# Kernel optimization log

Hardware: AMD Instinct MI355X
Metric: run time of the kernel (lower is better)

## Reference

```python
import jax, jax.numpy as jnp
import numpy as np

N_NODES = 10000
N_EDGES = 640000
IN_DIM, HID_DIM, OUT_DIM = 128, 512, 512


def setup_inputs() -> dict:
    key = jax.random.key(0)
    k1, k2, k3, k4, k5, k6 = jax.random.split(key, 6)
    feat = jax.random.normal(k1, (N_NODES, IN_DIM), dtype=jnp.float32)
    edge_index = jax.random.randint(k2, (2, N_EDGES), 0, N_NODES, dtype=jnp.int64)
    s1 = 1.0 / np.sqrt(IN_DIM)
    s2 = 1.0 / np.sqrt(HID_DIM)
    W1 = jax.random.uniform(k3, (IN_DIM, HID_DIM), jnp.float32, -s1, s1)
    b1 = jnp.zeros((HID_DIM,), jnp.float32)
    W2 = jax.random.uniform(k4, (HID_DIM, OUT_DIM), jnp.float32, -s2, s2)
    b2 = jnp.zeros((OUT_DIM,), jnp.float32)
    return {"feat": feat, "edge_index": edge_index, "W1": W1, "b1": b1, "W2": W2, "b2": b2}


def _degree_norms(edge_index, n_nodes):
    src, dst = edge_index[0], edge_index[1]
    ones = jnp.ones((edge_index.shape[1],), jnp.float32)
    out_deg = jax.ops.segment_sum(ones, src, num_segments=n_nodes)
    in_deg = jax.ops.segment_sum(ones, dst, num_segments=n_nodes)
    # DGL clamps degree to >= 1 to avoid division by zero
    norm_src = jax.lax.rsqrt(jnp.maximum(out_deg, 1.0))  # [N]
    norm_dst = jax.lax.rsqrt(jnp.maximum(in_deg, 1.0))   # [N]
    return norm_src, norm_dst


def _graph_conv(x, src, dst, norm_src, norm_dst, W, b, n_nodes):
    # norm='both': D_in^{-1/2} A D_out^{-1/2} X W + b
    x = x * norm_src[:, None]
    agg = jax.ops.segment_sum(x[src], dst, num_segments=n_nodes)  # [N, d]
    agg = agg * norm_dst[:, None]
    return agg @ W + b


def reference(feat, edge_index, W1, b1, W2, b2):
    n = feat.shape[0]
    src, dst = edge_index[0], edge_index[1]
    norm_src, norm_dst = _degree_norms(edge_index, n)
    h = _graph_conv(feat, src, dst, norm_src, norm_dst, W1, b1, n)
    h = jax.nn.relu(h)
    out = _graph_conv(h, src, dst, norm_src, norm_dst, W2, b2, n)
    return out
```

## Files before the change

kernel.cpp:

```cpp
#include <hip/hip_runtime.h>

#define NN 10000
#define NE 640000
#define IN_DIM 128
#define HID_DIM 512
#define OUT_DIM 512
#define NB 10240
#define P_PART 128
#define EPB (NE / P_PART)

typedef __attribute__((ext_vector_type(8))) short short8;
typedef __attribute__((ext_vector_type(4))) float f32x4;
typedef __attribute__((ext_vector_type(2))) float f32x2;

__device__ __forceinline__ ushort f2b(float f) {
    union { float f; uint i; } c; c.f = f;
    uint x = c.i;
    uint r = (x + 0x7fffu + ((x >> 16) & 1u)) >> 16;
    return (ushort)r;
}
__device__ __forceinline__ float blo(uint a) {
    union { uint i; float f; } c; c.i = a << 16; return c.f;
}
__device__ __forceinline__ float bhi(uint a) {
    union { uint i; float f; } c; c.i = a & 0xffff0000u; return c.f;
}

__device__ __forceinline__ void gl_lds16(const ushort* g, ushort* l) {
    __builtin_amdgcn_global_load_lds((const __attribute__((address_space(1))) uint*)g,
                                     (__attribute__((address_space(3))) uint*)l, 16, 0, 0);
}

__global__ __launch_bounds__(1024) void histw_kernel(const int* __restrict__ ei,
                                                     ushort* __restrict__ pcnt_dst,
                                                     ushort* __restrict__ pcnt_src,
                                                     const float* __restrict__ W1,
                                                     ushort* __restrict__ W1t,
                                                     const float* __restrict__ W2,
                                                     ushort* __restrict__ W2t) {
    __shared__ int h[NB];
    int b = blockIdx.x;
    int t = threadIdx.x;
    if (b < 256) {
        int p = b & 127;
        const int* __restrict__ idx = (b < 128) ? (ei + NE) : ei;
        ushort* __restrict__ outp = (b < 128) ? pcnt_dst : pcnt_src;
        for (int i = t; i < NB; i += 1024) h[i] = 0;
        __syncthreads();
        int base = p * EPB;
        for (int i = t; i < EPB; i += 1024) atomicAdd(&h[idx[base + i]], 1);
        __syncthreads();
        for (int i = t; i < NB; i += 1024) outp[p * NB + i] = (ushort)h[i];
        return;
    }
    float* tld = (float*)h;
    const float* W; ushort* Wt; int K, N, k0, n0;
    if (b < 320) {
        int bb = b - 256;
        W = W1; Wt = W1t; K = IN_DIM; N = HID_DIM;
        k0 = (bb & 3) * 32; n0 = (bb >> 2) * 32;
    } else {
        int bb = b - 320;
        W = W2; Wt = W2t; K = HID_DIM; N = OUT_DIM;
        k0 = (bb & 15) * 32; n0 = (bb >> 4) * 32;
    }
    int r = t >> 5, c = t & 31;
    tld[r * 33 + c] = W[(size_t)(k0 + r) * N + n0 + c];
    __syncthreads();
    Wt[(size_t)(n0 + r) * K + k0 + c] = f2b(tld[c * 33 + r]);
}

__global__ __launch_bounds__(256) void colreduce_kernel(const ushort* __restrict__ pcnt_dst,
                                                        const ushort* __restrict__ pcnt_src,
                                                        int* __restrict__ poff,
                                                        int* __restrict__ deg_in,
                                                        float* __restrict__ norm_src,
                                                        float* __restrict__ norm_dst) {
    int v = blockIdx.x * 256 + threadIdx.x;
    int s = 0;
#pragma unroll 4
    for (int p = 0; p < P_PART; p++) {
        int c = pcnt_dst[p * NB + v];
        poff[p * NB + v] = s;
        s += c;
    }
    deg_in[v] = s;
    int s2 = 0;
#pragma unroll 4
    for (int p = 0; p < P_PART; p++) s2 += pcnt_src[p * NB + v];
    if (v < NN) {
        norm_dst[v] = rsqrtf(fmaxf((float)s, 1.0f));
        norm_src[v] = rsqrtf(fmaxf((float)s2, 1.0f));
    }
}

__global__ __launch_bounds__(1024) void scanfeat_kernel(const int* __restrict__ deg,
                                                        int* __restrict__ row_off,
                                                        const float* __restrict__ feat,
                                                        const float* __restrict__ norm_src,
                                                        ushort* __restrict__ featb) {
    int b = blockIdx.x;
    int t = threadIdx.x;
    if (b == 0) {
        const int PER = NB / 1024;
        __shared__ int lds[1024];
        int base = t * PER;
        int local[PER];
        int s = 0;
#pragma unroll
        for (int i = 0; i < PER; i++) {
            int v = deg[base + i];
            local[i] = s;
            s += v;
        }
        lds[t] = s;
        __syncthreads();
        for (int off = 1; off < 1024; off <<= 1) {
            int x = (t >= off) ? lds[t - off] : 0;
            __syncthreads();
            lds[t] += x;
            __syncthreads();
        }
        int excl = lds[t] - s;
#pragma unroll
        for (int i = 0; i < PER; i++) {
            int idx = base + i;
            if (idx <= NN) row_off[idx] = excl + local[i];
        }
        return;
    }
    int i = (b - 1) * 1024 + t;
    if (i < NN * IN_DIM / 4) {
        float4 v = ((const float4*)feat)[i];
        float s = norm_src[i >> 5];
        ushort4 o;
        o.x = f2b(v.x * s); o.y = f2b(v.y * s); o.z = f2b(v.z * s); o.w = f2b(v.w * s);
        ((ushort4*)featb)[i] = o;
    }
}

__global__ __launch_bounds__(1024) void fill_kernel(const int* __restrict__ src,
                                                    const int* __restrict__ dst,
                                                    const int* __restrict__ row_off,
                                                    const int* __restrict__ poff,
                                                    int* __restrict__ csr_src) {
    __shared__ int cur[NB];
    int p = blockIdx.x, t = threadIdx.x;
    for (int i = t; i < NB; i += 1024)
        cur[i] = ((i < NN) ? row_off[i] : 0) + poff[p * NB + i];
    __syncthreads();
    int base = p * EPB;
    for (int i = t; i < EPB; i += 1024) {
        int d = dst[base + i];
        int slot = atomicAdd(&cur[d], 1);
        csr_src[slot] = src[base + i];
    }
}

__global__ __launch_bounds__(64) void agg1_kernel(const uint* __restrict__ fb,
                                                  const int* __restrict__ row_off,
                                                  const int* __restrict__ csr_src,
                                                  const float* __restrict__ norm_dst,
                                                  uint* __restrict__ aggb) {
    int node = blockIdx.x;
    uint lane = threadIdx.x;
    int beg = row_off[node], end = row_off[node + 1];
    f32x2 acc = {0.f, 0.f};
    int i = beg;
    for (; i + 8 <= end; i += 8) {
        const uint* rp[8];
#pragma unroll
        for (int j = 0; j < 8; j++)
            rp[j] = fb + (uint)__builtin_amdgcn_readfirstlane(csr_src[i + j]) * 64u;
        uint a[8];
#pragma unroll
        for (int j = 0; j < 8; j++) a[j] = rp[j][lane];
#pragma unroll
        for (int j = 0; j < 8; j++) {
            f32x2 v; v.x = blo(a[j]); v.y = bhi(a[j]);
            acc += v;
        }
    }
    for (; i < end; i++) {
        const uint* rp = fb + (uint)__builtin_amdgcn_readfirstlane(csr_src[i]) * 64u;
        uint a = rp[lane];
        f32x2 v; v.x = blo(a); v.y = bhi(a);
        acc += v;
    }
    float nd = norm_dst[node];
    aggb[node * 64 + lane] = (uint)f2b(acc.x * nd) | ((uint)f2b(acc.y * nd) << 16);
}

__global__ __launch_bounds__(64) void agg2_kernel(const uint* __restrict__ hb,
                                                  const int* __restrict__ row_off,
                                                  const int* __restrict__ csr_src,
                                                  const float* __restrict__ norm_dst,
                                                  uint* __restrict__ aggb) {
    int node = blockIdx.x;
    uint t = blockIdx.y * 64 + threadIdx.x;
    int beg = row_off[node], end = row_off[node + 1];
    f32x2 acc = {0.f, 0.f};
    int i = beg;
    for (; i + 8 <= end; i += 8) {
        const uint* rp[8];
#pragma unroll
        for (int j = 0; j < 8; j++)
            rp[j] = hb + (uint)__builtin_amdgcn_readfirstlane(csr_src[i + j]) * 256u;
        uint a[8];
#pragma unroll
        for (int j = 0; j < 8; j++) a[j] = rp[j][t];
#pragma unroll
        for (int j = 0; j < 8; j++) {
            f32x2 v; v.x = blo(a[j]); v.y = bhi(a[j]);
            acc += v;
        }
    }
    for (; i < end; i++) {
        const uint* rp = hb + (uint)__builtin_amdgcn_readfirstlane(csr_src[i]) * 256u;
        uint a = rp[t];
        f32x2 v; v.x = blo(a); v.y = bhi(a);
        acc += v;
    }
    float nd = norm_dst[node];
    aggb[node * 256 + t] = (uint)f2b(acc.x * nd) | ((uint)f2b(acc.y * nd) << 16);
}

template <int EPI>
__global__ __launch_bounds__(256) void gemm_bf16_kernel(const ushort* __restrict__ A,
                                                        const ushort* __restrict__ Bt,
                                                        const float* __restrict__ bias,
                                                        const float* __restrict__ scale,
                                                        void* __restrict__ Cout,
                                                        int M, int K, int N) {
    const int BM = 128;
    __shared__ __align__(16) ushort As[BM * 32];
    __shared__ __align__(16) ushort Bs[64 * 32];
    int tid = threadIdx.x;
    int lane = tid & 63;
    int wid = tid >> 6;
    int bm = blockIdx.x * BM;
    int bn = blockIdx.y * 64;
    int wm = (wid & 1) * 64;
    int wn = (wid >> 1) * 32;

    int cA0 = tid, cA1 = 256 + tid, cB = tid;
    int rowA0 = ((cA0 >> 6) << 4) | (cA0 & 15), kqA0 = (cA0 >> 4) & 3;
    int rowA1 = ((cA1 >> 6) << 4) | (cA1 & 15), kqA1 = (cA1 >> 4) & 3;
    int rowB = ((cB >> 6) << 4) | (cB & 15), kqB = (cB >> 4) & 3;
    const ushort* srcA0 = A + (size_t)(bm + rowA0) * K + kqA0 * 8;
    const ushort* srcA1 = A + (size_t)(bm + rowA1) * K + kqA1 * 8;
    const ushort* srcB = Bt + (size_t)(bn + rowB) * K + kqB * 8;
    ushort* ldsA0 = As + (wid * 64) * 8;
    ushort* ldsA1 = As + (256 + wid * 64) * 8;
    ushort* ldsB = Bs + (wid * 64) * 8;

    f32x4 acc[4][2] = {};

    for (int k0 = 0; k0 < K; k0 += 32) {
        __syncthreads();
        gl_lds16(srcA0 + k0, ldsA0);
        gl_lds16(srcA1 + k0, ldsA1);
        gl_lds16(srcB + k0, ldsB);
        __syncthreads();
        short8 af[4], bfr[2];
#pragma unroll
        for (int i = 0; i < 4; i++) {
            int j = (((wm >> 4) + i) << 6) + ((lane >> 4) << 4) + (lane & 15);
            af[i] = *(const short8*)(As + j * 8);
        }
#pragma unroll
        for (int i = 0; i < 2; i++) {
            int j = (((wn >> 4) + i) << 6) + ((lane >> 4) << 4) + (lane & 15);
            bfr[i] = *(const short8*)(Bs + j * 8);
        }
#pragma unroll
        for (int i = 0; i < 4; i++)
#pragma unroll
            for (int jn = 0; jn < 2; jn++)
                acc[i][jn] = __builtin_amdgcn_mfma_f32_16x16x32_bf16(af[i], bfr[jn], acc[i][jn], 0, 0, 0);
    }

#pragma unroll
    for (int i = 0; i < 4; i++) {
#pragma unroll
        for (int jn = 0; jn < 2; jn++) {
            int col = bn + wn + jn * 16 + (lane & 15);
            float bv = bias[col];
#pragma unroll
            for (int r = 0; r < 4; r++) {
                int gm = bm + wm + i * 16 + ((lane >> 4) << 2) + r;
                if (gm < M) {
                    float v = acc[i][jn][r] + bv;
                    if (EPI == 1) {
                        v = fmaxf(v, 0.f) * scale[gm];
                        ((ushort*)Cout)[(size_t)gm * N + col] = f2b(v);
                    } else {
                        ((float*)Cout)[(size_t)gm * N + col] = v;
                    }
                }
            }
        }
    }
}

extern "C" void kernel_launch(void* const* d_in, const int* in_sizes, int n_in,
                              void* d_out, int out_size, void* d_ws, size_t ws_size,
                              hipStream_t stream) {
    const float* feat = (const float*)d_in[0];
    const int* ei = (const int*)d_in[1];
    const float* W1 = (const float*)d_in[2];
    const float* b1 = (const float*)d_in[3];
    const float* W2 = (const float*)d_in[4];
    const float* b2 = (const float*)d_in[5];
    float* out = (float*)d_out;

    const int* src = ei;
    const int* dst = ei + NE;
    const int NNP = 10112;

    char* ws = (char*)d_ws;
    size_t off = 0;
    auto alloc = [&](size_t bytes) -> void* {
        void* p = ws + off;
        off += (bytes + 255) & ~(size_t)255;
        return p;
    };
    int* row_off = (int*)alloc((NN + 16) * sizeof(int));
    int* deg_in = (int*)alloc(NB * sizeof(int));
    float* norm_src = (float*)alloc(NN * sizeof(float));
    float* norm_dst = (float*)alloc(NN * sizeof(float));
    int* csr_src = (int*)alloc(NE * sizeof(int));
    ushort* featb = (ushort*)alloc((size_t)NN * IN_DIM * 2);
    ushort* W1t = (ushort*)alloc((size_t)HID_DIM * IN_DIM * 2);
    ushort* W2t = (ushort*)alloc((size_t)OUT_DIM * HID_DIM * 2);
    size_t union_base = off;
    ushort* pcnt_dst = (ushort*)alloc((size_t)P_PART * NB * sizeof(ushort));
    ushort* pcnt_src = (ushort*)alloc((size_t)P_PART * NB * sizeof(ushort));
    int* poff = (int*)alloc((size_t)P_PART * NB * sizeof(int));
    off = union_base;
    ushort* agg1b = (ushort*)alloc((size_t)NNP * IN_DIM * 2);
    ushort* hb = (ushort*)alloc((size_t)NN * HID_DIM * 2);
    ushort* agg2b = (ushort*)alloc((size_t)NNP * HID_DIM * 2);

    histw_kernel<<<576, 1024, 0, stream>>>(ei, pcnt_dst, pcnt_src, W1, W1t, W2, W2t);
    colreduce_kernel<<<NB / 256, 256, 0, stream>>>(pcnt_dst, pcnt_src, poff, deg_in, norm_src, norm_dst);
    scanfeat_kernel<<<314, 1024, 0, stream>>>(deg_in, row_off, feat, norm_src, featb);
    fill_kernel<<<P_PART, 1024, 0, stream>>>(src, dst, row_off, poff, csr_src);

    agg1_kernel<<<NN, 64, 0, stream>>>((const uint*)featb, row_off, csr_src, norm_dst, (uint*)agg1b);
    {
        dim3 grid(NNP / 128, HID_DIM / 64);
        gemm_bf16_kernel<1><<<grid, 256, 0, stream>>>(agg1b, W1t, b1, norm_src, hb, NN, IN_DIM, HID_DIM);
    }
    {
        dim3 grid(NN, 4);
        agg2_kernel<<<grid, 64, 0, stream>>>((const uint*)hb, row_off, csr_src, norm_dst, (uint*)agg2b);
    }
    {
        dim3 grid(NNP / 128, OUT_DIM / 64);
        gemm_bf16_kernel<0><<<grid, 256, 0, stream>>>(agg2b, W2t, b2, nullptr, out, NN, HID_DIM, OUT_DIM);
    }
}
```

Baseline: 136.3 us.

## Split wavefront across two edges in aggregation and double-buffer 128x128 GEMM tiles

The two aggregation kernels become one template in which each half-wavefront gathers a different neighbour edge with 8-byte loads. The halves are combined with a cross-lane shuffle, which doubles the number of rows in flight per load instruction. The GEMM tile grows from 128x64 to 128x128 with a double-buffered LDS pipeline, so the next K-slice is prefetched while MFMAs run, and one barrier per iteration is removed. The cost is more LDS and registers per block, fewer GEMM blocks (which lowers occupancy), and a partially idle wavefront at the end of odd-degree rows.

```diff
diff --git a/kernel.cpp b/kernel.cpp
--- a/kernel.cpp
+++ b/kernel.cpp
@@ -157,72 +157,56 @@
     }
 }
 
-__global__ __launch_bounds__(64) void agg1_kernel(const uint* __restrict__ fb,
-                                                  const int* __restrict__ row_off,
-                                                  const int* __restrict__ csr_src,
-                                                  const float* __restrict__ norm_dst,
-                                                  uint* __restrict__ aggb) {
+template <int ROWU>
+__global__ __launch_bounds__(64) void agg_kernel(const uint* __restrict__ tab,
+                                                 const int* __restrict__ row_off,
+                                                 const int* __restrict__ csr_src,
+                                                 const float* __restrict__ norm_dst,
+                                                 uint* __restrict__ outb) {
     int node = blockIdx.x;
+    uint soff = blockIdx.y * 64u;
     uint lane = threadIdx.x;
+    uint half = lane >> 5;
+    uint lq = (lane & 31u) * 2u + soff;
     int beg = row_off[node], end = row_off[node + 1];
-    f32x2 acc = {0.f, 0.f};
+    f32x4 acc = {0.f, 0.f, 0.f, 0.f};
     int i = beg;
     for (; i + 8 <= end; i += 8) {
-        const uint* rp[8];
-#pragma unroll
-        for (int j = 0; j < 8; j++)
-            rp[j] = fb + (uint)__builtin_amdgcn_readfirstlane(csr_src[i + j]) * 64u;
-        uint a[8];
-#pragma unroll
-        for (int j = 0; j < 8; j++) a[j] = rp[j][lane];
-#pragma unroll
-        for (int j = 0; j < 8; j++) {
-            f32x2 v; v.x = blo(a[j]); v.y = bhi(a[j]);
+        uint2 a[4];
+#pragma unroll
+        for (int j = 0; j < 4; j++) {
+            uint u = (uint)csr_src[i + 2 * j + half];
+            a[j] = *(const uint2*)(tab + u * (uint)ROWU + lq);
+        }
+#pragma unroll
+        for (int j = 0; j < 4; j++) {
+            f32x4 v; v.x = blo(a[j].x); v.y = bhi(a[j].x); v.z = blo(a[j].y); v.w = bhi(a[j].y);
             acc += v;
         }
     }
-    for (; i < end; i++) {
-        const uint* rp = fb + (uint)__builtin_amdgcn_readfirstlane(csr_src[i]) * 64u;
-        uint a = rp[lane];
-        f32x2 v; v.x = blo(a); v.y = bhi(a);
+    for (; i + 2 <= end; i += 2) {
+        uint u = (uint)csr_src[i + half];
+        uint2 a = *(const uint2*)(tab + u * (uint)ROWU + lq);
+        f32x4 v; v.x = blo(a.x); v.y = bhi(a.x); v.z = blo(a.y); v.w = bhi(a.y);
         acc += v;
     }
-    float nd = norm_dst[node];
-    aggb[node * 64 + lane] = (uint)f2b(acc.x * nd) | ((uint)f2b(acc.y * nd) << 16);
-}
-
-__global__ __launch_bounds__(64) void agg2_kernel(const uint* __restrict__ hb,
-                                                  const int* __restrict__ row_off,
-                                                  const int* __restrict__ csr_src,
-                                                  const float* __restrict__ norm_dst,
-                                                  uint* __restrict__ aggb) {
-    int node = blockIdx.x;
-    uint t = blockIdx.y * 64 + threadIdx.x;
-    int beg = row_off[node], end = row_off[node + 1];
-    f32x2 acc = {0.f, 0.f};
-    int i = beg;
-    for (; i + 8 <= end; i += 8) {
-        const uint* rp[8];
-#pragma unroll
-        for (int j = 0; j < 8; j++)
-            rp[j] = hb + (uint)__builtin_amdgcn_readfirstlane(csr_src[i + j]) * 256u;
-        uint a[8];
-#pragma unroll
-        for (int j = 0; j < 8; j++) a[j] = rp[j][t];
-#pragma unroll
-        for (int j = 0; j < 8; j++) {
-            f32x2 v; v.x = blo(a[j]); v.y = bhi(a[j]);
-            acc += v;
-        }
-    }
-    for (; i < end; i++) {
-        const uint* rp = hb + (uint)__builtin_amdgcn_readfirstlane(csr_src[i]) * 256u;
-        uint a = rp[t];
-        f32x2 v; v.x = blo(a); v.y = bhi(a);
+    if (i < end && half == 0) {
+        uint u = (uint)csr_src[i];
+        uint2 a = *(const uint2*)(tab + u * (uint)ROWU + lq);
+        f32x4 v; v.x = blo(a.x); v.y = bhi(a.x); v.z = blo(a.y); v.w = bhi(a.y);
         acc += v;
     }
-    float nd = norm_dst[node];
-    aggb[node * 256 + t] = (uint)f2b(acc.x * nd) | ((uint)f2b(acc.y * nd) << 16);
+    acc.x += __shfl_down(acc.x, 32);
+    acc.y += __shfl_down(acc.y, 32);
+    acc.z += __shfl_down(acc.z, 32);
+    acc.w += __shfl_down(acc.w, 32);
+    if (lane < 32) {
+        float nd = norm_dst[node];
+        uint2 o;
+        o.x = (uint)f2b(acc.x * nd) | ((uint)f2b(acc.y * nd) << 16);
+        o.y = (uint)f2b(acc.z * nd) | ((uint)f2b(acc.w * nd) << 16);
+        *(uint2*)(outb + (uint)node * (uint)ROWU + lq) = o;
+    }
 }
 
 template <int EPI>
@@ -232,58 +216,71 @@
                                                         const float* __restrict__ scale,
                                                         void* __restrict__ Cout,
                                                         int M, int K, int N) {
-    const int BM = 128;
-    __shared__ __align__(16) ushort As[BM * 32];
-    __shared__ __align__(16) ushort Bs[64 * 32];
+    __shared__ __align__(16) ushort As[2][128 * 32];
+    __shared__ __align__(16) ushort Bs[2][128 * 32];
     int tid = threadIdx.x;
     int lane = tid & 63;
     int wid = tid >> 6;
-    int bm = blockIdx.x * BM;
-    int bn = blockIdx.y * 64;
+    int bm = blockIdx.x * 128;
+    int bn = blockIdx.y * 128;
     int wm = (wid & 1) * 64;
-    int wn = (wid >> 1) * 32;
-
-    int cA0 = tid, cA1 = 256 + tid, cB = tid;
-    int rowA0 = ((cA0 >> 6) << 4) | (cA0 & 15), kqA0 = (cA0 >> 4) & 3;
-    int rowA1 = ((cA1 >> 6) << 4) | (cA1 & 15), kqA1 = (cA1 >> 4) & 3;
-    int rowB = ((cB >> 6) << 4) | (cB & 15), kqB = (cB >> 4) & 3;
-    const ushort* srcA0 = A + (size_t)(bm + rowA0) * K + kqA0 * 8;
-    const ushort* srcA1 = A + (size_t)(bm + rowA1) * K + kqA1 * 8;
-    const ushort* srcB = Bt + (size_t)(bn + rowB) * K + kqB * 8;
-    ushort* ldsA0 = As + (wid * 64) * 8;
-    ushort* ldsA1 = As + (256 + wid * 64) * 8;
-    ushort* ldsB = Bs + (wid * 64) * 8;
-
-    f32x4 acc[4][2] = {};
-
-    for (int k0 = 0; k0 < K; k0 += 32) {
-        __syncthreads();
-        gl_lds16(srcA0 + k0, ldsA0);
-        gl_lds16(srcA1 + k0, ldsA1);
-        gl_lds16(srcB + k0, ldsB);
-        __syncthreads();
-        short8 af[4], bfr[2];
+    int wn = (wid >> 1) * 64;
+
+    int c0 = tid, c1 = 256 + tid;
+    int row0 = ((c0 >> 6) << 4) | (c0 & 15), kq0 = (c0 >> 4) & 3;
+    int row1 = ((c1 >> 6) << 4) | (c1 & 15), kq1 = (c1 >> 4) & 3;
+    const ushort* sA0 = A + (size_t)(bm + row0) * K + kq0 * 8;
+    const ushort* sA1 = A + (size_t)(bm + row1) * K + kq1 * 8;
+    const ushort* sB0 = Bt + (size_t)(bn + row0) * K + kq0 * 8;
+    const ushort* sB1 = Bt + (size_t)(bn + row1) * K + kq1 * 8;
+    uint lo0 = (uint)(wid * 64) * 8u;
+    uint lo1 = (uint)(256 + wid * 64) * 8u;
+
+    f32x4 acc[4][4] = {};
+
+    const int NT = K / 32;
+    gl_lds16(sA0, &As[0][lo0]);
+    gl_lds16(sA1, &As[0][lo1]);
+    gl_lds16(sB0, &Bs[0][lo0]);
+    gl_lds16(sB1, &Bs[0][lo1]);
+    __syncthreads();
+
+    int cur = 0;
+    for (int t = 0; t < NT; t++) {
+        if (t + 1 < NT) {
+            int kn = (t + 1) * 32;
+            gl_lds16(sA0 + kn, &As[cur ^ 1][lo0]);
+            gl_lds16(sA1 + kn, &As[cur ^ 1][lo1]);
+            gl_lds16(sB0 + kn, &Bs[cur ^ 1][lo0]);
+            gl_lds16(sB1 + kn, &Bs[cur ^ 1][lo1]);
+        }
+        short8 af[4], bfr[4];
+        int fo = ((lane >> 4) << 4) + (lane & 15);
 #pragma unroll
         for (int i = 0; i < 4; i++) {
-            int j = (((wm >> 4) + i) << 6) + ((lane >> 4) << 4) + (lane & 15);
-            af[i] = *(const short8*)(As + j * 8);
-        }
-#pragma unroll
-        for (int i = 0; i < 2; i++) {
-            int j = (((wn >> 4) + i) << 6) + ((lane >> 4) << 4) + (lane & 15);
-            bfr[i] = *(const short8*)(Bs + j * 8);
+            int j = (((wm >> 4) + i) << 6) + fo;
+            af[i] = *(const short8*)(&As[cur][j * 8]);
+        }
+#pragma unroll
+        for (int i = 0; i < 4; i++) {
+            int j = (((wn >> 4) + i) << 6) + fo;
+            bfr[i] = *(const short8*)(&Bs[cur][j * 8]);
         }
 #pragma unroll
         for (int i = 0; i < 4; i++)
 #pragma unroll
-            for (int jn = 0; jn < 2; jn++)
+            for (int jn = 0; jn < 4; jn++)
                 acc[i][jn] = __builtin_amdgcn_mfma_f32_16x16x32_bf16(af[i], bfr[jn], acc[i][jn], 0, 0, 0);
+        if (t + 1 < NT) {
+            __syncthreads();
+            cur ^= 1;
+        }
     }
 
 #pragma unroll
     for (int i = 0; i < 4; i++) {
 #pragma unroll
-        for (int jn = 0; jn < 2; jn++) {
+        for (int jn = 0; jn < 4; jn++) {
             int col = bn + wn + jn * 16 + (lane & 15);
             float bv = bias[col];
 #pragma unroll
@@ -347,17 +344,20 @@
     scanfeat_kernel<<<314, 1024, 0, stream>>>(deg_in, row_off, feat, norm_src, featb);
     fill_kernel<<<P_PART, 1024, 0, stream>>>(src, dst, row_off, poff, csr_src);
 
-    agg1_kernel<<<NN, 64, 0, stream>>>((const uint*)featb, row_off, csr_src, norm_dst, (uint*)agg1b);
     {
-        dim3 grid(NNP / 128, HID_DIM / 64);
+        dim3 grid(NN, 1);
+        agg_kernel<64><<<grid, 64, 0, stream>>>((const uint*)featb, row_off, csr_src, norm_dst, (uint*)agg1b);
+    }
+    {
+        dim3 grid(NNP / 128, HID_DIM / 128);
         gemm_bf16_kernel<1><<<grid, 256, 0, stream>>>(agg1b, W1t, b1, norm_src, hb, NN, IN_DIM, HID_DIM);
     }
     {
         dim3 grid(NN, 4);
-        agg2_kernel<<<grid, 64, 0, stream>>>((const uint*)hb, row_off, csr_src, norm_dst, (uint*)agg2b);
+        agg_kernel<256><<<grid, 64, 0, stream>>>((const uint*)hb, row_off, csr_src, norm_dst, (uint*)agg2b);
     }
     {
-        dim3 grid(NNP / 128, OUT_DIM / 64);
+        dim3 grid(NNP / 128, OUT_DIM / 128);
         gemm_bf16_kernel<0><<<grid, 256, 0, stream>>>(agg2b, W2t, b2, nullptr, out, NN, HID_DIM, OUT_DIM);
     }
 }
```

After: 158.5 us. 1.16x slower.
